# Performance work log

Measured on AMD Instinct MI355X. Metric: run time of the kernel, lower is better.

## Reference

```python
import jax, jax.numpy as jnp
import numpy as np

N_ROLES = 6
EPS = 1e-5

def _ln(x, scale, bias):
    m = jnp.mean(x, axis=-1, keepdims=True)
    v = jnp.var(x, axis=-1, keepdims=True)
    return (x - m) * jax.lax.rsqrt(v + EPS) * scale + bias

def setup_inputs() -> dict:
    key = jax.random.key(0)
    ks = jax.random.split(key, 20)
    T, B, D_OBS, H, A = 32, 1024, 256, 512, 32
    inp = {
        'rnn_states': jax.random.normal(ks[0], (B, H), jnp.float32),
        'obs': jax.random.normal(ks[1], (T, B, D_OBS), jnp.float32),
        'resets': jnp.zeros((T, B), jnp.float32),
        'available_actions': jnp.ones((T, B, A), jnp.float32),
        'role_ids': jax.random.randint(ks[2], (T, B), 0, N_ROLES, jnp.int32),
        # feature norm over obs_dim
        'fn_scale': jnp.ones((D_OBS,), jnp.float32),
        'fn_bias': jnp.zeros((D_OBS,), jnp.float32),
        # base MLP: obs_dim->512->512, each followed by LayerNorm
        'W0': jax.random.normal(ks[3], (D_OBS, H), jnp.float32) * 0.02,
        'b0': jnp.zeros((H,), jnp.float32),
        'ln0_scale': jnp.ones((H,), jnp.float32),
        'ln0_bias': jnp.zeros((H,), jnp.float32),
        'W1': jax.random.normal(ks[4], (H, H), jnp.float32) * 0.02,
        'b1': jnp.zeros((H,), jnp.float32),
        'ln1_scale': jnp.ones((H,), jnp.float32),
        'ln1_bias': jnp.zeros((H,), jnp.float32),
        # per-role routes: obs_dim->128->H (stacked over roles)
        'Wr0': jax.random.normal(ks[5], (N_ROLES, D_OBS, 128), jnp.float32) * 0.02,
        'br0': jnp.zeros((N_ROLES, 128), jnp.float32),
        'Wr1': jax.random.normal(ks[6], (N_ROLES, 128, H), jnp.float32) * 0.02,
        'br1': jnp.zeros((N_ROLES, H), jnp.float32),
        # per-role heads: H->64->32->action_dim (stacked over roles)
        'Wh0': jax.random.normal(ks[7], (N_ROLES, H, 64), jnp.float32) * 0.02,
        'bh0': jnp.zeros((N_ROLES, 64), jnp.float32),
        'Wh1': jax.random.normal(ks[8], (N_ROLES, 64, 32), jnp.float32) * 0.02,
        'bh1': jnp.zeros((N_ROLES, 32), jnp.float32),
        'Wh2': jax.random.normal(ks[9], (N_ROLES, 32, A), jnp.float32) * 0.02,
        'bh2': jnp.zeros((N_ROLES, A), jnp.float32),
    }
    return inp

def _gather_by_role(all_values, role_ids):
    # all_values: (K, T, B, F); role_ids: (T, B) -> (T, B, F)
    idx = role_ids[None, :, :, None].astype(jnp.int32)
    return jnp.take_along_axis(all_values, idx, axis=0)[0]

def reference(rnn_states, obs, resets, available_actions, role_ids,
              fn_scale, fn_bias, W0, b0, ln0_scale, ln0_bias,
              W1, b1, ln1_scale, ln1_bias,
              Wr0, br0, Wr1, br1,
              Wh0, bh0, Wh1, bh1, Wh2, bh2):
    # feature normalization on raw obs
    obs_n = _ln(obs, fn_scale, fn_bias)
    # shared base MLP (relu + LayerNorm after each Dense)
    e = _ln(jax.nn.relu(obs_n @ W0 + b0), ln0_scale, ln0_bias)
    e = _ln(jax.nn.relu(e @ W1 + b1), ln1_scale, ln1_bias)
    # per-role pre-GRU residual routes on (normalized) obs
    r = jax.nn.relu(jnp.einsum('tbi,kih->ktbh', obs_n, Wr0) + br0[:, None, None, :])
    r = jax.nn.relu(jnp.einsum('ktbh,kho->ktbo', r, Wr1) + br1[:, None, None, :])
    e = e + _gather_by_role(r, role_ids)
    # no recurrent policy configured: rnn_states pass through
    # per-role heads -> all logits (K, T, B, A)
    h = jax.nn.relu(jnp.einsum('tbh,khf->ktbf', e, Wh0) + bh0[:, None, None, :])
    h = jax.nn.relu(jnp.einsum('ktbf,kfg->ktbg', h, Wh1) + bh1[:, None, None, :])
    all_logits = jnp.einsum('ktbg,kga->ktba', h, Wh2) + bh2[:, None, None, :]
    logits = _gather_by_role(all_logits, role_ids)
    logits = jnp.where(available_actions > 0.5, logits, jnp.full_like(logits, -1e10))
    return rnn_states, logits
```

## Files before the change

kernel.cpp:

```cpp
#include <hip/hip_runtime.h>
#include <stdint.h>

typedef unsigned short u16;
typedef unsigned int u32;

using bf16x8 = __attribute__((ext_vector_type(8))) short;
using f32x4  = __attribute__((ext_vector_type(4))) float;

#define DEVINL __device__ __forceinline__

DEVINL float b2f(u16 u) { return __builtin_bit_cast(float, (u32)u << 16); }
DEVINL u16 f2b(float f) {
  u32 u = __builtin_bit_cast(u32, f);
  u += 0x7FFFu + ((u >> 16) & 1u);
  return (u16)(u >> 16);
}

DEVINL void gll16(const u16* src, u16* dst) {
  __builtin_amdgcn_global_load_lds(
      (const __attribute__((address_space(1))) void*)(uintptr_t)src,
      (__attribute__((address_space(3))) void*)(uintptr_t)dst, 16, 0, 0);
}

#define MFMA __builtin_amdgcn_mfma_f32_16x16x32_bf16
#define NROLE 6

DEVINL void tp_tile(const float* __restrict__ s, u16* __restrict__ d,
                    int R, int C, int bx, int by, int z)
{
  __shared__ u16 tile[32][33];
  const size_t mstride = (size_t)R * C;
  s += (size_t)z * mstride;
  d += (size_t)z * mstride;
  int r0 = bx * 32, c0 = by * 32;
  int tx = threadIdx.x & 31, ty = threadIdx.x >> 5;
#pragma unroll
  for (int i = 0; i < 32; i += 8)
    tile[ty + i][tx] = f2b(s[(size_t)(r0 + ty + i) * C + (c0 + tx)]);
  __syncthreads();
#pragma unroll
  for (int i = 0; i < 32; i += 8)
    d[(size_t)(c0 + ty + i) * R + (r0 + tx)] = tile[tx][ty + i];
}

__global__ __launch_bounds__(256) void mega0(
    const float* W0, const float* W1, const float* Wr0, const float* Wr1, const float* Wh0,
    u16* W0t, u16* W1t, u16* Wr0t, u16* Wr1t, u16* Wh0t,
    const float* __restrict__ obs, const float* __restrict__ fn_s,
    const float* __restrict__ fn_b, u16* __restrict__ obs_n,
    const int* __restrict__ rid, int* __restrict__ blkCnt,
    const float* __restrict__ rnn, float* __restrict__ outRnn)
{
  int b = blockIdx.x;
  const int tid = threadIdx.x;
  if (b < 1152) {
    if (b < 128)      {            tp_tile(W0, W0t, 256, 512, b % 8,  b / 8, 0); }
    else if (b < 384) { b -= 128;  tp_tile(W1, W1t, 512, 512, b % 16, b / 16, 0); }
    else if (b < 576) { b -= 384;  int t = b / 8;  tp_tile(Wr0, Wr0t, 256, 128, b % 8,  t % 4,  t / 4); }
    else if (b < 960) { b -= 576;  int t = b / 4;  tp_tile(Wr1, Wr1t, 128, 512, b % 4,  t % 16, t / 16); }
    else              { b -= 960;  int t = b / 16; tp_tile(Wh0, Wh0t, 512, 64,  b % 16, t % 2,  t / 2); }
  } else if (b < 3200) {
    b -= 1152;
    const int lane = tid & 63, wave = tid >> 6;
#pragma unroll
    for (int it = 0; it < 4; ++it) {
      int row = b * 16 + wave * 4 + it;
      const float* xr = obs + (size_t)row * 256 + lane * 4;
      float x[4] __attribute__((aligned(16)));
      *(float4*)x = *(const float4*)xr;
      float s = 0.f, s2 = 0.f;
#pragma unroll
      for (int p = 0; p < 4; ++p) { s += x[p]; s2 += x[p] * x[p]; }
#pragma unroll
      for (int o = 32; o > 0; o >>= 1) { s += __shfl_xor(s, o, 64); s2 += __shfl_xor(s2, o, 64); }
      float m = s * (1.f / 256.f);
      float v = s2 * (1.f / 256.f) - m * m;
      float inv = rsqrtf(v + 1e-5f);
      u16 yu[4] __attribute__((aligned(8)));
#pragma unroll
      for (int p = 0; p < 4; ++p)
        yu[p] = f2b((x[p] - m) * inv * fn_s[lane * 4 + p] + fn_b[lane * 4 + p]);
      *(uint2*)(obs_n + (size_t)row * 256 + lane * 4) = *(uint2*)yu;
    }
  } else if (b < 3328) {
    b -= 3200;
    __shared__ int h[NROLE];
    if (tid < NROLE) h[tid] = 0;
    __syncthreads();
    atomicAdd(&h[rid[b * 256 + tid]], 1);
    __syncthreads();
    if (tid < NROLE) blkCnt[b * NROLE + tid] = h[tid];
  } else {
    b -= 3328;
    const float4* src = (const float4*)rnn;
    float4* dst = (float4*)outRnn;
    int base = (b * 256 + tid) * 4;
#pragma unroll
    for (int i = 0; i < 4; ++i) dst[base + i] = src[base + i];
  }
}

__global__ __launch_bounds__(256) void fill2(
    const int* __restrict__ rid, const int* __restrict__ blkCnt,
    int* __restrict__ bucket, int* __restrict__ baseArr, int* __restrict__ cntArr)
{
  __shared__ int c[128 * NROLE];
  __shared__ int preArr[NROLE], scnt[NROLE], sbase[NROLE], h[NROLE];
  const int tid = threadIdx.x;
  const int bx = blockIdx.x;
  for (int i = tid; i < 128 * NROLE; i += 256) c[i] = blkCnt[i];
  if (tid < NROLE) h[tid] = 0;
  __syncthreads();
  if (tid < NROLE) {
    int k = tid, run = 0, pre = 0;
    for (int b = 0; b < 128; ++b) { if (b == bx) pre = run; run += c[b * NROLE + k]; }
    scnt[k] = run; preArr[k] = pre;
  }
  __syncthreads();
  if (tid == 0) {
    int r = 0;
    for (int k = 0; k < NROLE; ++k) { sbase[k] = r; r += scnt[k]; }
  }
  __syncthreads();
  if (bx == 0 && tid < NROLE) { baseArr[tid] = sbase[tid]; cntArr[tid] = scnt[tid]; }
  int i = bx * 256 + tid;
  int k = rid[i];
  int pos = atomicAdd(&h[k], 1);
  bucket[sbase[k] + preArr[k] + pos] = i;
}

template <int K>
__global__ __launch_bounds__(256, 2) void gemm_ln(
    const u16* __restrict__ A, const u16* __restrict__ Bt,
    const float* __restrict__ bias, const float* __restrict__ lnsc,
    const float* __restrict__ lnbi, u16* __restrict__ C)
{
  constexpr int BK = 128, NI = K / BK, NC = K / 32;
  __shared__ __align__(16) u16 As[2][64 * BK];
  __shared__ float redS[64][4];
  __shared__ float redSS[64][4];
  __shared__ float prm[1536];
  const int tid = threadIdx.x;
  const int rowBase = blockIdx.x * 64;
  const int lane = tid & 63, wave = tid >> 6;
#pragma unroll
  for (int i = tid; i < 512; i += 256) {
    prm[i] = bias[i]; prm[512 + i] = lnsc[i]; prm[1024 + i] = lnbi[i];
  }
  u32 aOff[4];
#pragma unroll
  for (int r = 0; r < 4; ++r) {
    int row = r * 16 + (tid >> 4);
    int chunk = tid & 15;
    aOff[r] = (u32)(rowBase + row) * (u32)K + (u32)((chunk ^ (row & 7)) * 8);
  }
  const int quad = lane >> 4, lm = lane & 15, l7 = lm & 7;
  const int wn = wave * 128;
  u32 bOff[8];
#pragma unroll
  for (int j = 0; j < 8; ++j)
    bOff[j] = (u32)(wn + j * 16 + lm) * (u32)K + (u32)(quad * 8);

  f32x4 acc[4][8] = {};

#pragma unroll
  for (int r = 0; r < 4; ++r)
    gll16(A + aOff[r], &As[0][r * 2048 + wave * 512]);
  bf16x8 bP[8];
#pragma unroll
  for (int j = 0; j < 8; ++j)
    bP[j] = *(const bf16x8*)(Bt + bOff[j]);
  __syncthreads();

  for (int i = 0; i < NI; ++i) {
    const u16* Ab = As[i & 1];
    if (i + 1 < NI) {
#pragma unroll
      for (int r = 0; r < 4; ++r)
        gll16(A + aOff[r] + (i + 1) * BK, &As[(i + 1) & 1][r * 2048 + wave * 512]);
    }
#pragma unroll
    for (int c = 0; c < 4; ++c) {
      const int g = i * 4 + c;
      bf16x8 bN[8];
      if (g + 1 < NC) {
#pragma unroll
        for (int j = 0; j < 8; ++j)
          bN[j] = *(const bf16x8*)(Bt + bOff[j] + (g + 1) * 32);
      }
      const int kc = c * 4;
      bf16x8 af[4];
#pragma unroll
      for (int i2 = 0; i2 < 4; ++i2)
        af[i2] = *(const bf16x8*)&Ab[(i2 * 16 + lm) * BK + (((quad + kc) ^ l7) * 8)];
#pragma unroll
      for (int i2 = 0; i2 < 4; ++i2)
#pragma unroll
        for (int j = 0; j < 8; ++j)
          acc[i2][j] = MFMA(af[i2], bP[j], acc[i2][j], 0, 0, 0);
      if (g + 1 < NC) {
#pragma unroll
        for (int j = 0; j < 8; ++j) bP[j] = bN[j];
      }
    }
    __syncthreads();
  }

#pragma unroll
  for (int i2 = 0; i2 < 4; ++i2) {
#pragma unroll
    for (int r2 = 0; r2 < 4; ++r2) {
      float s = 0.f, ss = 0.f;
#pragma unroll
      for (int j = 0; j < 8; ++j) {
        float v = fmaxf(acc[i2][j][r2] + prm[wn + j * 16 + lm], 0.f);
        acc[i2][j][r2] = v;
        s += v; ss += v * v;
      }
#pragma unroll
      for (int o = 1; o < 16; o <<= 1) { s += __shfl_xor(s, o, 64); ss += __shfl_xor(ss, o, 64); }
      if (lm == 0) {
        int rowL = i2 * 16 + quad * 4 + r2;
        redS[rowL][wave] = s;
        redSS[rowL][wave] = ss;
      }
    }
  }
  __syncthreads();
#pragma unroll
  for (int i2 = 0; i2 < 4; ++i2) {
#pragma unroll
    for (int r2 = 0; r2 < 4; ++r2) {
      int rowL = i2 * 16 + quad * 4 + r2;
      float ts  = redS[rowL][0] + redS[rowL][1] + redS[rowL][2] + redS[rowL][3];
      float tss = redSS[rowL][0] + redSS[rowL][1] + redSS[rowL][2] + redSS[rowL][3];
      float m = ts * (1.f / 512.f);
      float var = tss * (1.f / 512.f) - m * m;
      float inv = rsqrtf(var + 1e-5f);
      size_t base = (size_t)(rowBase + rowL) * 512;
#pragma unroll
      for (int j = 0; j < 8; ++j) {
        int col = wn + j * 16 + lm;
        float y = (acc[i2][j][r2] - m) * inv * prm[512 + col] + prm[1024 + col];
        C[base + col] = f2b(y);
      }
    }
  }
}

__global__ __launch_bounds__(256, 4) void route_head(
    const u16* __restrict__ obs_n, const u16* __restrict__ e,
    const u16* __restrict__ Wr0t, const float* __restrict__ br0,
    const u16* __restrict__ Wr1t, const float* __restrict__ br1,
    const u16* __restrict__ Wh0t, const float* __restrict__ bh0,
    const float* __restrict__ Wh1, const float* __restrict__ bh1,
    const float* __restrict__ Wh2, const float* __restrict__ bh2,
    const float* __restrict__ avail,
    const int* __restrict__ bucket, const int* __restrict__ baseArr,
    const int* __restrict__ cntArr, float* __restrict__ outLogits)
{
  __shared__ __align__(16) u16 sm[20480];
  const int tid = threadIdx.x;

  int cA0, cA1, cA2, cA3, cA4, cA5, bA0, bA1, bA2, bA3, bA4, bA5;
  {
    int4 ca = *(const int4*)cntArr;  int2 cb = *(const int2*)(cntArr + 4);
    int4 ba = *(const int4*)baseArr; int2 bb = *(const int2*)(baseArr + 4);
    cA0 = ca.x; cA1 = ca.y; cA2 = ca.z; cA3 = ca.w; cA4 = cb.x; cA5 = cb.y;
    bA0 = ba.x; bA1 = ba.y; bA2 = ba.z; bA3 = ba.w; bA4 = bb.x; bA5 = bb.y;
  }
  int role = -1, rem = blockIdx.x, cnt = 0, roleBase = 0;
#define TRY_ROLE(k, ck, bk)                                        \
  if (role < 0) {                                                  \
    int tiles = ((ck) + 31) >> 5;                                  \
    if (rem < tiles) { role = (k); cnt = (ck); roleBase = (bk); }  \
    else rem -= tiles;                                             \
  }
  TRY_ROLE(0, cA0, bA0) TRY_ROLE(1, cA1, bA1) TRY_ROLE(2, cA2, bA2)
  TRY_ROLE(3, cA3, bA3) TRY_ROLE(4, cA4, bA4) TRY_ROLE(5, cA5, bA5)
#undef TRY_ROLE
  if (role < 0) return;
  const int limit = cnt;
  const int rowBase = rem * 32;

  const int lane = tid & 63, wave = tid >> 6;
  const int quad = lane >> 4, lm = lane & 15, l7 = lm & 7;

#pragma unroll
  for (int r = 0; r < 8; ++r) {
    int lrow = r * 4 + wave;
    int i = rowBase + lrow;
    if (i >= limit) i = rowBase;
    int grow = bucket[roleBase + i];
    int chunk = tid & 63;
    int sw = (chunk & 56) | ((chunk ^ lrow) & 7);
    gll16(e + (u32)grow * 512u + (u32)(sw * 8), &sm[r * 2048 + wave * 512]);
  }

  int growA0, growA1;
  {
    int i0 = rowBase + lm;        if (i0 >= limit) i0 = rowBase;
    int i1 = rowBase + 16 + lm;   if (i1 >= limit) i1 = rowBase;
    growA0 = bucket[roleBase + i0];
    growA1 = bucket[roleBase + i1];
  }
  const u16* Ag0 = obs_n + (size_t)growA0 * 256;
  const u16* Ag1 = obs_n + (size_t)growA1 * 256;

  const int wn0 = wave * 32;
  const u16* B0 = Wr0t + (size_t)role * 128 * 256;
  f32x4 acc0[2][2] = {};
  bf16x8 b0R[2][2];
#pragma unroll
  for (int p = 0; p < 2; ++p)
#pragma unroll
    for (int j = 0; j < 2; ++j)
      b0R[p][j] = *(const bf16x8*)(B0 + (u32)(wn0 + j * 16 + lm) * 256u + (u32)(quad * 8 + p * 32));
  bf16x8 aR[4][2];
#pragma unroll
  for (int p = 0; p < 4; ++p) {
    aR[p][0] = *(const bf16x8*)(Ag0 + (u32)(quad * 8 + p * 32));
    aR[p][1] = *(const bf16x8*)(Ag1 + (u32)(quad * 8 + p * 32));
  }
  float bias0[2] = { br0[role * 128 + wn0 + lm], br0[role * 128 + wn0 + 16 + lm] };
#pragma unroll
  for (int it = 0; it < 8; ++it) {
    bf16x8 a0 = aR[it & 3][0], a1 = aR[it & 3][1];
    bf16x8 cur0 = b0R[it & 1][0], cur1 = b0R[it & 1][1];
    if (it + 2 < 8) {
#pragma unroll
      for (int j = 0; j < 2; ++j)
        b0R[it & 1][j] = *(const bf16x8*)(B0 + (u32)(wn0 + j * 16 + lm) * 256u + (u32)(quad * 8 + (it + 2) * 32));
    }
    if (it + 4 < 8) {
      aR[it & 3][0] = *(const bf16x8*)(Ag0 + (u32)(quad * 8 + (it + 4) * 32));
      aR[it & 3][1] = *(const bf16x8*)(Ag1 + (u32)(quad * 8 + (it + 4) * 32));
    }
    acc0[0][0] = MFMA(a0, cur0, acc0[0][0], 0, 0, 0);
    acc0[0][1] = MFMA(a0, cur1, acc0[0][1], 0, 0, 0);
    acc0[1][0] = MFMA(a1, cur0, acc0[1][0], 0, 0, 0);
    acc0[1][1] = MFMA(a1, cur1, acc0[1][1], 0, 0, 0);
  }
  u16* r1 = sm + 16384;
#pragma unroll
  for (int i2 = 0; i2 < 2; ++i2) {
#pragma unroll
    for (int r2 = 0; r2 < 4; ++r2) {
      int row = i2 * 16 + quad * 4 + r2;
#pragma unroll
      for (int j = 0; j < 2; ++j) {
        int col = wn0 + j * 16 + lm;
        float v = fmaxf(acc0[i2][j][r2] + bias0[j], 0.f);
        r1[row * 128 + (((col >> 3) ^ (row & 7)) * 8) + (col & 7)] = f2b(v);
      }
    }
  }
  const int wn1 = wave * 128;
  float b1v[8];
#pragma unroll
  for (int j = 0; j < 8; ++j) b1v[j] = br1[role * 512 + wn1 + j * 16 + lm];
  __syncthreads();

  const u16* B1 = Wr1t + (size_t)role * 512 * 128;
  f32x4 acc1[2][8] = {};
  bf16x8 b1P[8];
#pragma unroll
  for (int j = 0; j < 8; ++j)
    b1P[j] = *(const bf16x8*)(B1 + (u32)(wn1 + j * 16 + lm) * 128u + (u32)(quad * 8));
#pragma unroll
  for (int kk = 0; kk < 128; kk += 32) {
    bf16x8 b1N[8];
    if (kk + 32 < 128) {
#pragma unroll
      for (int j = 0; j < 8; ++j)
        b1N[j] = *(const bf16x8*)(B1 + (u32)(wn1 + j * 16 + lm) * 128u + (u32)(quad * 8 + kk + 32));
    }
    const int kc = kk >> 3;
    bf16x8 af[2];
#pragma unroll
    for (int i2 = 0; i2 < 2; ++i2)
      af[i2] = *(const bf16x8*)&r1[(i2 * 16 + lm) * 128 + (((quad + kc) ^ l7) * 8)];
#pragma unroll
    for (int i2 = 0; i2 < 2; ++i2)
#pragma unroll
      for (int j = 0; j < 8; ++j)
        acc1[i2][j] = MFMA(af[i2], b1P[j], acc1[i2][j], 0, 0, 0);
    if (kk + 32 < 128) {
#pragma unroll
      for (int j = 0; j < 8; ++j) b1P[j] = b1N[j];
    }
  }
#pragma unroll
  for (int i2 = 0; i2 < 2; ++i2) {
#pragma unroll
    for (int r2 = 0; r2 < 4; ++r2) {
      int row = i2 * 16 + quad * 4 + r2;
#pragma unroll
      for (int j = 0; j < 8; ++j) {
        int col = wn1 + j * 16 + lm;
        int addr = row * 512 + (((col >> 3) ^ (row & 7)) * 8) + (col & 7);
        float v = fmaxf(acc1[i2][j][r2] + b1v[j], 0.f) + b2f(sm[addr]);
        sm[addr] = f2b(v);
      }
    }
  }
  __syncthreads();

  const int wn2 = wave * 16;
  const u16* B2 = Wh0t + (size_t)role * 64 * 512;
  float b2v = bh0[role * 64 + wn2 + lm];
  f32x4 acc2[2] = {};
  bf16x8 b2R[4];
#pragma unroll
  for (int p = 0; p < 4; ++p)
    b2R[p] = *(const bf16x8*)(B2 + (u32)(wn2 + lm) * 512u + (u32)(quad * 8 + p * 32));
#pragma unroll
  for (int it = 0; it < 16; ++it) {
    bf16x8 cur = b2R[it & 3];
    if (it + 4 < 16)
      b2R[it & 3] = *(const bf16x8*)(B2 + (u32)(wn2 + lm) * 512u + (u32)(quad * 8 + (it + 4) * 32));
    const int kc = it * 4;
    bf16x8 af[2];
#pragma unroll
    for (int i2 = 0; i2 < 2; ++i2)
      af[i2] = *(const bf16x8*)&sm[(i2 * 16 + lm) * 512 + (((quad + kc) ^ l7) * 8)];
#pragma unroll
    for (int i2 = 0; i2 < 2; ++i2)
      acc2[i2] = MFMA(af[i2], cur, acc2[i2], 0, 0, 0);
  }
  u16* h0s = sm + 16384;
#pragma unroll
  for (int i2 = 0; i2 < 2; ++i2) {
#pragma unroll
    for (int r2 = 0; r2 < 4; ++r2) {
      int row = i2 * 16 + quad * 4 + r2;
      int col = wn2 + lm;
      h0s[row * 68 + col] = f2b(fmaxf(acc2[i2][r2] + b2v, 0.f));
    }
  }
  __syncthreads();

  {
    float* h1s = (float*)&sm[16384];
    const int r = tid >> 3;
    const int n0 = (tid & 7) * 4;
    const bool valid = (rowBase + r) < limit;
    const float* W1k = Wh1 + (size_t)role * 64 * 32;
    const float* W2k = Wh2 + (size_t)role * 32 * 32;
    float4 a1 = *(const float4*)(bh1 + role * 32 + n0);
#pragma unroll 8
    for (int j = 0; j < 64; ++j) {
      float hj = b2f(h0s[r * 68 + j]);
      float4 wv = *(const float4*)(W1k + j * 32 + n0);
      a1.x += hj * wv.x; a1.y += hj * wv.y; a1.z += hj * wv.z; a1.w += hj * wv.w;
    }
    a1.x = fmaxf(a1.x, 0.f); a1.y = fmaxf(a1.y, 0.f);
    a1.z = fmaxf(a1.z, 0.f); a1.w = fmaxf(a1.w, 0.f);
    __syncthreads();
    h1s[r * 36 + n0 + 0] = a1.x;
    h1s[r * 36 + n0 + 1] = a1.y;
    h1s[r * 36 + n0 + 2] = a1.z;
    h1s[r * 36 + n0 + 3] = a1.w;
    __syncthreads();
    float4 a2 = *(const float4*)(bh2 + role * 32 + n0);
#pragma unroll 8
    for (int n = 0; n < 32; ++n) {
      float hn = h1s[r * 36 + n];
      float4 wv = *(const float4*)(W2k + n * 32 + n0);
      a2.x += hn * wv.x; a2.y += hn * wv.y; a2.z += hn * wv.z; a2.w += hn * wv.w;
    }
    if (valid) {
      int g = bucket[roleBase + rowBase + r];
      float4 av = *(const float4*)(avail + (size_t)g * 32 + n0);
      float4 o;
      o.x = (av.x > 0.5f) ? a2.x : -1e10f;
      o.y = (av.y > 0.5f) ? a2.y : -1e10f;
      o.z = (av.z > 0.5f) ? a2.z : -1e10f;
      o.w = (av.w > 0.5f) ? a2.w : -1e10f;
      *(float4*)(outLogits + (size_t)g * 32 + n0) = o;
    }
  }
}

extern "C" void kernel_launch(void* const* d_in, const int* in_sizes, int n_in,
                              void* d_out, int out_size, void* d_ws, size_t ws_size,
                              hipStream_t stream)
{
  const float* rnn  = (const float*)d_in[0];
  const float* obs  = (const float*)d_in[1];
  const float* avail= (const float*)d_in[3];
  const int*   rid  = (const int*)d_in[4];
  const float* fn_s = (const float*)d_in[5];
  const float* fn_b = (const float*)d_in[6];
  const float* W0   = (const float*)d_in[7];
  const float* b0   = (const float*)d_in[8];
  const float* ln0s = (const float*)d_in[9];
  const float* ln0b = (const float*)d_in[10];
  const float* W1   = (const float*)d_in[11];
  const float* b1   = (const float*)d_in[12];
  const float* ln1s = (const float*)d_in[13];
  const float* ln1b = (const float*)d_in[14];
  const float* Wr0  = (const float*)d_in[15];
  const float* br0  = (const float*)d_in[16];
  const float* Wr1  = (const float*)d_in[17];
  const float* br1  = (const float*)d_in[18];
  const float* Wh0  = (const float*)d_in[19];
  const float* bh0  = (const float*)d_in[20];
  const float* Wh1  = (const float*)d_in[21];
  const float* bh1  = (const float*)d_in[22];
  const float* Wh2  = (const float*)d_in[23];
  const float* bh2  = (const float*)d_in[24];

  const int ROWS = 32768;

  char* w = (char*)d_ws;
  auto carve = [&](size_t bytes) { char* p = w; w += (bytes + 255) & ~(size_t)255; return p; };
  u16* obs_n  = (u16*)carve((size_t)ROWS * 256 * 2);
  u16* bufA   = (u16*)carve((size_t)ROWS * 512 * 2);
  u16* bufB   = (u16*)carve((size_t)ROWS * 512 * 2);
  u16* W0t    = (u16*)carve((size_t)512 * 256 * 2);
  u16* W1t    = (u16*)carve((size_t)512 * 512 * 2);
  u16* Wr0t   = (u16*)carve((size_t)6 * 128 * 256 * 2);
  u16* Wr1t   = (u16*)carve((size_t)6 * 512 * 128 * 2);
  u16* Wh0t   = (u16*)carve((size_t)6 * 64 * 512 * 2);
  int* bucket = (int*)carve((size_t)ROWS * 4);
  int* blkCnt = (int*)carve((size_t)128 * NROLE * 4);
  int* baseArr= (int*)carve(256);
  int* cntArr = (int*)carve(256);

  float* outLogits = (float*)d_out + (size_t)1024 * 512;

  mega0<<<3456, 256, 0, stream>>>(W0, W1, Wr0, Wr1, Wh0, W0t, W1t, Wr0t, Wr1t, Wh0t,
                                  obs, fn_s, fn_b, obs_n, rid, blkCnt, rnn, (float*)d_out);

  fill2<<<128, 256, 0, stream>>>(rid, blkCnt, bucket, baseArr, cntArr);

  gemm_ln<256><<<512, 256, 0, stream>>>(obs_n, W0t, b0, ln0s, ln0b, bufA);
  gemm_ln<512><<<512, 256, 0, stream>>>(bufA, W1t, b1, ln1s, ln1b, bufB);

  route_head<<<1029, 256, 0, stream>>>(obs_n, bufB, Wr0t, br0, Wr1t, br1, Wh0t, bh0,
                                       Wh1, bh1, Wh2, bh2, avail,
                                       bucket, baseArr, cntArr, outLogits);
}
```

Baseline: 290.1 us.

## Fuse second base GEMM and LayerNorm into per-role route/head kernel

Removes the separate gemm_ln<512> launch and its intermediate buffer. The route kernel now gathers rows of the first-layer output, runs the 512x512 W1 GEMM with bias, ReLU and LayerNorm in shared memory, and then continues with the route and head stages. This saves a launch and a full write and re-read of the 32768x512 bf16 intermediate. In exchange, shared memory grows to about 73KB and launch bounds drop to 2 blocks per SM, so occupancy falls. Each 32-row tile also streams the whole W1 matrix from cache with a small M tile, which may reduce GEMM efficiency.

```diff
diff --git a/kernel.cpp b/kernel.cpp
--- a/kernel.cpp
+++ b/kernel.cpp
@@ -248,8 +248,10 @@
   }
 }
 
-__global__ __launch_bounds__(256, 4) void route_head(
-    const u16* __restrict__ obs_n, const u16* __restrict__ e,
+__global__ __launch_bounds__(256, 2) void route_all(
+    const u16* __restrict__ obs_n, const u16* __restrict__ eA,
+    const u16* __restrict__ W1t, const float* __restrict__ b1,
+    const float* __restrict__ ln1sc, const float* __restrict__ ln1bi,
     const u16* __restrict__ Wr0t, const float* __restrict__ br0,
     const u16* __restrict__ Wr1t, const float* __restrict__ br1,
     const u16* __restrict__ Wh0t, const float* __restrict__ bh0,
@@ -259,7 +261,7 @@
     const int* __restrict__ bucket, const int* __restrict__ baseArr,
     const int* __restrict__ cntArr, float* __restrict__ outLogits)
 {
-  __shared__ __align__(16) u16 sm[20480];
+  __shared__ __align__(16) u16 sm[37376];
   const int tid = threadIdx.x;
 
   int cA0, cA1, cA2, cA3, cA4, cA5, bA0, bA1, bA2, bA3, bA4, bA5;
@@ -294,7 +296,7 @@
     int grow = bucket[roleBase + i];
     int chunk = tid & 63;
     int sw = (chunk & 56) | ((chunk ^ lrow) & 7);
-    gll16(e + (u32)grow * 512u + (u32)(sw * 8), &sm[r * 2048 + wave * 512]);
+    gll16(eA + (u32)grow * 512u + (u32)(sw * 8), &sm[r * 2048 + wave * 512]);
   }
 
   int growA0, growA1;
@@ -341,7 +343,7 @@
     acc0[1][0] = MFMA(a1, cur0, acc0[1][0], 0, 0, 0);
     acc0[1][1] = MFMA(a1, cur1, acc0[1][1], 0, 0, 0);
   }
-  u16* r1 = sm + 16384;
+  u16* r1 = sm + 32768;
 #pragma unroll
   for (int i2 = 0; i2 < 2; ++i2) {
 #pragma unroll
@@ -355,52 +357,143 @@
       }
     }
   }
-  const int wn1 = wave * 128;
-  float b1v[8];
-#pragma unroll
-  for (int j = 0; j < 8; ++j) b1v[j] = br1[role * 512 + wn1 + j * 16 + lm];
-  __syncthreads();
-
-  const u16* B1 = Wr1t + (size_t)role * 512 * 128;
+  __syncthreads();
+
+  const int wn = wave * 128;
+  u32 bOffW[8];
+#pragma unroll
+  for (int j = 0; j < 8; ++j)
+    bOffW[j] = (u32)(wn + j * 16 + lm) * 512u + (u32)(quad * 8);
+  f32x4 accE[2][8] = {};
+  {
+    bf16x8 bR[2][8];
+#pragma unroll
+    for (int p = 0; p < 2; ++p)
+#pragma unroll
+      for (int j = 0; j < 8; ++j)
+        bR[p][j] = *(const bf16x8*)(W1t + bOffW[j] + p * 32);
+#pragma unroll
+    for (int g = 0; g < 16; ++g) {
+      bf16x8 cur[8];
+#pragma unroll
+      for (int j = 0; j < 8; ++j) cur[j] = bR[g & 1][j];
+      if (g + 2 < 16) {
+#pragma unroll
+        for (int j = 0; j < 8; ++j)
+          bR[g & 1][j] = *(const bf16x8*)(W1t + bOffW[j] + (g + 2) * 32);
+      }
+      const int kc = g * 4;
+      bf16x8 af[2];
+#pragma unroll
+      for (int i2 = 0; i2 < 2; ++i2)
+        af[i2] = *(const bf16x8*)&sm[(i2 * 16 + lm) * 512 + (((quad + kc) ^ l7) * 8)];
+#pragma unroll
+      for (int i2 = 0; i2 < 2; ++i2)
+#pragma unroll
+        for (int j = 0; j < 8; ++j)
+          accE[i2][j] = MFMA(af[i2], cur[j], accE[i2][j], 0, 0, 0);
+    }
+  }
+  float* redS  = (float*)&sm[36864];
+  float* redSS = redS + 128;
+  {
+    float b1v[8];
+#pragma unroll
+    for (int j = 0; j < 8; ++j) b1v[j] = b1[wn + j * 16 + lm];
+#pragma unroll
+    for (int i2 = 0; i2 < 2; ++i2) {
+#pragma unroll
+      for (int r2 = 0; r2 < 4; ++r2) {
+        float s = 0.f, ss = 0.f;
+#pragma unroll
+        for (int j = 0; j < 8; ++j) {
+          float v = fmaxf(accE[i2][j][r2] + b1v[j], 0.f);
+          accE[i2][j][r2] = v;
+          s += v; ss += v * v;
+        }
+#pragma unroll
+        for (int o = 1; o < 16; o <<= 1) { s += __shfl_xor(s, o, 64); ss += __shfl_xor(ss, o, 64); }
+        if (lm == 0) {
+          int row = i2 * 16 + quad * 4 + r2;
+          redS[row * 4 + wave] = s;
+          redSS[row * 4 + wave] = ss;
+        }
+      }
+    }
+  }
+  __syncthreads();
+  {
+    float lsv[8], lbv[8];
+#pragma unroll
+    for (int j = 0; j < 8; ++j) {
+      lsv[j] = ln1sc[wn + j * 16 + lm];
+      lbv[j] = ln1bi[wn + j * 16 + lm];
+    }
+#pragma unroll
+    for (int i2 = 0; i2 < 2; ++i2) {
+#pragma unroll
+      for (int r2 = 0; r2 < 4; ++r2) {
+        int row = i2 * 16 + quad * 4 + r2;
+        float ts  = redS[row * 4 + 0] + redS[row * 4 + 1] + redS[row * 4 + 2] + redS[row * 4 + 3];
+        float tss = redSS[row * 4 + 0] + redSS[row * 4 + 1] + redSS[row * 4 + 2] + redSS[row * 4 + 3];
+        float m = ts * (1.f / 512.f);
+        float var = tss * (1.f / 512.f) - m * m;
+        float inv = rsqrtf(var + 1e-5f);
+#pragma unroll
+        for (int j = 0; j < 8; ++j) {
+          int col = wn + j * 16 + lm;
+          float y = (accE[i2][j][r2] - m) * inv * lsv[j] + lbv[j];
+          sm[16384 + row * 512 + (((col >> 3) ^ (row & 7)) * 8) + (col & 7)] = f2b(y);
+        }
+      }
+    }
+  }
+
+  const u16* B1r = Wr1t + (size_t)role * 512 * 128;
   f32x4 acc1[2][8] = {};
-  bf16x8 b1P[8];
-#pragma unroll
-  for (int j = 0; j < 8; ++j)
-    b1P[j] = *(const bf16x8*)(B1 + (u32)(wn1 + j * 16 + lm) * 128u + (u32)(quad * 8));
-#pragma unroll
-  for (int kk = 0; kk < 128; kk += 32) {
-    bf16x8 b1N[8];
-    if (kk + 32 < 128) {
-#pragma unroll
-      for (int j = 0; j < 8; ++j)
-        b1N[j] = *(const bf16x8*)(B1 + (u32)(wn1 + j * 16 + lm) * 128u + (u32)(quad * 8 + kk + 32));
-    }
-    const int kc = kk >> 3;
-    bf16x8 af[2];
-#pragma unroll
-    for (int i2 = 0; i2 < 2; ++i2)
-      af[i2] = *(const bf16x8*)&r1[(i2 * 16 + lm) * 128 + (((quad + kc) ^ l7) * 8)];
-#pragma unroll
-    for (int i2 = 0; i2 < 2; ++i2)
-#pragma unroll
-      for (int j = 0; j < 8; ++j)
-        acc1[i2][j] = MFMA(af[i2], b1P[j], acc1[i2][j], 0, 0, 0);
-    if (kk + 32 < 128) {
-#pragma unroll
-      for (int j = 0; j < 8; ++j) b1P[j] = b1N[j];
-    }
-  }
-#pragma unroll
-  for (int i2 = 0; i2 < 2; ++i2) {
-#pragma unroll
-    for (int r2 = 0; r2 < 4; ++r2) {
-      int row = i2 * 16 + quad * 4 + r2;
-#pragma unroll
-      for (int j = 0; j < 8; ++j) {
-        int col = wn1 + j * 16 + lm;
-        int addr = row * 512 + (((col >> 3) ^ (row & 7)) * 8) + (col & 7);
-        float v = fmaxf(acc1[i2][j][r2] + b1v[j], 0.f) + b2f(sm[addr]);
-        sm[addr] = f2b(v);
+  {
+    float b1v[8];
+#pragma unroll
+    for (int j = 0; j < 8; ++j) b1v[j] = br1[role * 512 + wn + j * 16 + lm];
+    bf16x8 b1P[8];
+#pragma unroll
+    for (int j = 0; j < 8; ++j)
+      b1P[j] = *(const bf16x8*)(B1r + (u32)(wn + j * 16 + lm) * 128u + (u32)(quad * 8));
+#pragma unroll
+    for (int kk = 0; kk < 128; kk += 32) {
+      bf16x8 b1N[8];
+      if (kk + 32 < 128) {
+#pragma unroll
+        for (int j = 0; j < 8; ++j)
+          b1N[j] = *(const bf16x8*)(B1r + (u32)(wn + j * 16 + lm) * 128u + (u32)(quad * 8 + kk + 32));
+      }
+      const int kc = kk >> 3;
+      bf16x8 af[2];
+#pragma unroll
+      for (int i2 = 0; i2 < 2; ++i2)
+        af[i2] = *(const bf16x8*)&r1[(i2 * 16 + lm) * 128 + (((quad + kc) ^ l7) * 8)];
+#pragma unroll
+      for (int i2 = 0; i2 < 2; ++i2)
+#pragma unroll
+        for (int j = 0; j < 8; ++j)
+          acc1[i2][j] = MFMA(af[i2], b1P[j], acc1[i2][j], 0, 0, 0);
+      if (kk + 32 < 128) {
+#pragma unroll
+        for (int j = 0; j < 8; ++j) b1P[j] = b1N[j];
+      }
+    }
+#pragma unroll
+    for (int i2 = 0; i2 < 2; ++i2) {
+#pragma unroll
+      for (int r2 = 0; r2 < 4; ++r2) {
+        int row = i2 * 16 + quad * 4 + r2;
+#pragma unroll
+        for (int j = 0; j < 8; ++j) {
+          int col = wn + j * 16 + lm;
+          int addr = 16384 + row * 512 + (((col >> 3) ^ (row & 7)) * 8) + (col & 7);
+          float v = fmaxf(acc1[i2][j][r2] + b1v[j], 0.f) + b2f(sm[addr]);
+          sm[addr] = f2b(v);
+        }
       }
     }
   }
@@ -423,12 +516,12 @@
     bf16x8 af[2];
 #pragma unroll
     for (int i2 = 0; i2 < 2; ++i2)
-      af[i2] = *(const bf16x8*)&sm[(i2 * 16 + lm) * 512 + (((quad + kc) ^ l7) * 8)];
+      af[i2] = *(const bf16x8*)&sm[16384 + (i2 * 16 + lm) * 512 + (((quad + kc) ^ l7) * 8)];
 #pragma unroll
     for (int i2 = 0; i2 < 2; ++i2)
       acc2[i2] = MFMA(af[i2], cur, acc2[i2], 0, 0, 0);
   }
-  u16* h0s = sm + 16384;
+  u16* h0s = sm + 32768;
 #pragma unroll
   for (int i2 = 0; i2 < 2; ++i2) {
 #pragma unroll
@@ -441,7 +534,7 @@
   __syncthreads();
 
   {
-    float* h1s = (float*)&sm[16384];
+    float* h1s = (float*)&sm[32768];
     const int r = tid >> 3;
     const int n0 = (tid & 7) * 4;
     const bool valid = (rowBase + r) < limit;
@@ -517,7 +610,6 @@
   auto carve = [&](size_t bytes) { char* p = w; w += (bytes + 255) & ~(size_t)255; return p; };
   u16* obs_n  = (u16*)carve((size_t)ROWS * 256 * 2);
   u16* bufA   = (u16*)carve((size_t)ROWS * 512 * 2);
-  u16* bufB   = (u16*)carve((size_t)ROWS * 512 * 2);
   u16* W0t    = (u16*)carve((size_t)512 * 256 * 2);
   u16* W1t    = (u16*)carve((size_t)512 * 512 * 2);
   u16* Wr0t   = (u16*)carve((size_t)6 * 128 * 256 * 2);
@@ -536,9 +628,9 @@
   fill2<<<128, 256, 0, stream>>>(rid, blkCnt, bucket, baseArr, cntArr);
 
   gemm_ln<256><<<512, 256, 0, stream>>>(obs_n, W0t, b0, ln0s, ln0b, bufA);
-  gemm_ln<512><<<512, 256, 0, stream>>>(bufA, W1t, b1, ln1s, ln1b, bufB);
-
-  route_head<<<1029, 256, 0, stream>>>(obs_n, bufB, Wr0t, br0, Wr1t, br1, Wh0t, bh0,
-                                       Wh1, bh1, Wh2, bh2, avail,
-                                       bucket, baseArr, cntArr, outLogits);
-}
+
+  route_all<<<1029, 256, 0, stream>>>(obs_n, bufA, W1t, b1, ln1s, ln1b,
+                                      Wr0t, br0, Wr1t, br1, Wh0t, bh0,
+                                      Wh1, bh1, Wh2, bh2, avail,
+                                      bucket, baseArr, cntArr, outLogits);
+}
```

Result: slower. 302.8 us (+4.4%).
